# Kernel tuning notes

Measured on AMD Instinct MI355X. Metric: run time of the kernel, lower is better.

## Reference

```python
import jax, jax.numpy as jnp
import numpy as np

NUM_QUBITS = 12
NUM_LAYERS = 2
STATE_DIM = 2 ** NUM_QUBITS
BATCH = 4096
TWO_PI = 2 * 3.1416  # matches the original initializer constant


def _u3(theta, phi, lam):
    """Single-qubit U3 gate, 2x2 complex64 (matches TF layer exactly)."""
    c = jnp.cos(theta / 2)
    s = jnp.sin(theta / 2)
    z = jnp.zeros_like(phi)
    e_phi = jnp.exp(jax.lax.complex(z, phi))
    e_lam = jnp.exp(jax.lax.complex(z, lam))
    e_pl = jnp.exp(jax.lax.complex(z, phi + lam))
    cc = jax.lax.complex(c, jnp.zeros_like(c))
    sc = jax.lax.complex(s, jnp.zeros_like(s))
    row1 = jnp.stack([cc, -e_lam * sc])
    row2 = jnp.stack([e_phi * sc, e_pl * cc])
    return jnp.stack([row1, row2])  # [2, 2] complex64


def _full_gate(theta_vec, phi_vec, lam_vec):
    """Kronecker product of per-qubit gates -> [2^n, 2^n] complex64."""
    full = _u3(theta_vec[0], phi_vec[0], lam_vec[0])
    for q in range(1, theta_vec.shape[0]):
        full = jnp.kron(full, _u3(theta_vec[q], phi_vec[q], lam_vec[q]))
    return full


def setup_inputs() -> dict:
    key = jax.random.key(0)
    k1, k2, k3, k4 = jax.random.split(key, 4)
    inputs = jax.random.normal(k1, (BATCH, STATE_DIM), dtype=jnp.float32)
    thetas = jax.random.uniform(k2, (NUM_LAYERS, NUM_QUBITS), minval=0.0, maxval=TWO_PI, dtype=jnp.float32)
    phis = jax.random.uniform(k3, (NUM_LAYERS, NUM_QUBITS), minval=0.0, maxval=TWO_PI, dtype=jnp.float32)
    lams = jax.random.uniform(k4, (NUM_LAYERS, NUM_QUBITS), minval=0.0, maxval=TWO_PI, dtype=jnp.float32)
    return {"inputs": inputs, "thetas": thetas, "phis": phis, "lams": lams}


def reference(inputs, thetas, phis, lams):
    # normalize real inputs as complex state, per-sample L2 norm
    state = jax.lax.complex(inputs, jnp.zeros_like(inputs))  # [B, D] complex64
    norm = jnp.linalg.norm(state, axis=1, keepdims=True)      # real, [B, 1]
    state = state / norm
    for l in range(thetas.shape[0]):
        U = _full_gate(thetas[l], phis[l], lams[l])  # [D, D]
        # matvec(U, x) per sample == state @ U^T, batched GEMM replaces tf.map_fn
        state = state @ U.T
    return jnp.real(state * jnp.conj(state))  # probabilities, [B, D] float32
```

## Files before the change

kernel.cpp:

```cpp
#include <hip/hip_runtime.h>
#include <hip/hip_fp16.h>

#define NQ   12
#define DIM  4096
#define NL   2
#define BATCH 4096

typedef _Float16 half8  __attribute__((ext_vector_type(8)));
typedef float    f32x16 __attribute__((ext_vector_type(16)));
typedef __fp16   hv2    __attribute__((ext_vector_type(2)));


union U4H8 { uint4 u; half8 h; };

__device__ __forceinline__ unsigned pkrtz(float a, float b) {
    union { hv2 h; unsigned u; } c;
    c.h = __builtin_amdgcn_cvt_pkrtz(a, b);
    return c.u;
}

__global__ void build_gates(const float* __restrict__ th,
                            const float* __restrict__ ph,
                            const float* __restrict__ lm,
                            unsigned short* __restrict__ ws) {
    __shared__ float g[12][8];
    int t = threadIdx.x;
    if (t < NQ) {
        int q = t;
        float g00r = 1.f, g00i = 0.f, g01r = 0.f, g01i = 0.f;
        float g10r = 0.f, g10i = 0.f, g11r = 1.f, g11i = 0.f;
        #pragma unroll
        for (int l = 0; l < NL; ++l) {
            float th2 = 0.5f * th[l * NQ + q];
            float p   = ph[l * NQ + q];
            float la  = lm[l * NQ + q];
            float s, c, sl, cl, sp, cp, spl, cpl;
            sincosf(th2, &s, &c);
            sincosf(la, &sl, &cl);
            sincosf(p, &sp, &cp);
            sincosf(p + la, &spl, &cpl);
            float u00r = c,        u00i = 0.f;
            float u01r = -cl * s,  u01i = -sl * s;
            float u10r = cp * s,   u10i = sp * s;
            float u11r = cpl * c,  u11i = spl * c;
            float n00r = u00r*g00r - u00i*g00i + u01r*g10r - u01i*g10i;
            float n00i = u00r*g00i + u00i*g00r + u01r*g10i + u01i*g10r;
            float n01r = u00r*g01r - u00i*g01i + u01r*g11r - u01i*g11i;
            float n01i = u00r*g01i + u00i*g01r + u01r*g11i + u01i*g11r;
            float n10r = u10r*g00r - u10i*g00i + u11r*g10r - u11i*g10i;
            float n10i = u10r*g00i + u10i*g00r + u11r*g10i + u11i*g10r;
            float n11r = u10r*g01r - u10i*g01i + u11r*g11r - u11i*g11i;
            float n11i = u10r*g01i + u10i*g01r + u11r*g11i + u11i*g11r;
            g00r = n00r; g00i = n00i; g01r = n01r; g01i = n01i;
            g10r = n10r; g10i = n10i; g11r = n11r; g11i = n11i;
        }
        g[q][0] = g00r; g[q][1] = g00i; g[q][2] = g01r; g[q][3] = g01i;
        g[q][4] = g10r; g[q][5] = g10i; g[q][6] = g11r; g[q][7] = g11i;
    }
    __syncthreads();

    for (int idx = t; idx < 24576; idx += 256) {
        int arr  = idx >> 13;
        int rem  = idx & 8191;
        int frag = rem >> 9;
        int lane = (rem >> 3) & 63;
        int j    = rem & 7;
        int row, col, base, k, nn = 0;
        if (arr == 0) {
            int n4 = frag >> 2, ks = frag & 3;
            nn  = n4 * 32 + (lane & 31);
            k   = ks * 16 + ((lane >> 5) << 3) + j;
            row = nn & 63; col = k; base = 6;
        } else {
            int m = frag >> 3, ks = frag & 7;
            row = m * 32 + (lane & 31);
            k   = ks * 16 + ((lane >> 5) << 3) + j;
            col = k & 63; base = 0;
        }
        float re = 1.f, im = 0.f;
        #pragma unroll
        for (int qq = 0; qq < 6; ++qq) {
            const float* G = g[base + qq];
            int rb = (row >> (5 - qq)) & 1;
            int cb = (col >> (5 - qq)) & 1;
            float fr = G[rb * 4 + cb * 2], fi = G[rb * 4 + cb * 2 + 1];
            float nre = re * fr - im * fi;
            float nim = re * fi + im * fr;
            re = nre; im = nim;
        }
        float val;
        if (arr == 0)      val = (nn < 64) ? re : im;
        else if (arr == 1) val = (k < 64) ? re : -im;
        else               val = (k < 64) ? im :  re;
        union { __fp16 h; unsigned short s; } cv;
        cv.h = (__fp16)val;
        ws[idx] = cv.s;
    }
}

__global__ __launch_bounds__(256, 2)
void qc_sim(const float* __restrict__ in,
            const unsigned short* __restrict__ gw,
            float* __restrict__ out) {
    __shared__ unsigned Xh32[2048];
    __shared__ unsigned Tc32[4096];
    __shared__ float red[4];

    const int t = threadIdx.x, lane = t & 63, w = t >> 6, b = blockIdx.x;
    const int m1 = w & 1, ng = (w >> 1) * 2;
    const int m2 = w & 1, n2 = w >> 1;

    const uint4* __restrict__ wsv = reinterpret_cast<const uint4*>(gw);
    uint4 g1b[2][4], m1f[8], m2f[8];
    #pragma unroll
    for (int n = 0; n < 2; ++n)
        #pragma unroll
        for (int ks = 0; ks < 4; ++ks)
            g1b[n][ks] = wsv[((ng + n) * 4 + ks) * 64 + lane];
    #pragma unroll
    for (int ks = 0; ks < 8; ++ks) m1f[ks] = wsv[1024 + (m2 * 8 + ks) * 64 + lane];
    #pragma unroll
    for (int ks = 0; ks < 8; ++ks) m2f[ks] = wsv[2048 + (m2 * 8 + ks) * 64 + lane];

    const float4* __restrict__ x4 =
        reinterpret_cast<const float4*>(in + (size_t)b * DIM);
    float4 lX[4];
    #pragma unroll
    for (int j = 0; j < 4; ++j) lX[j] = x4[j * 256 + t];

    float ss = 0.f;
    #pragma unroll
    for (int j = 0; j < 4; ++j)
        ss += lX[j].x*lX[j].x + lX[j].y*lX[j].y + lX[j].z*lX[j].z + lX[j].w*lX[j].w;
    #pragma unroll
    for (int off = 32; off > 0; off >>= 1) ss += __shfl_down(ss, off, 64);
    if (lane == 0) red[w] = ss;

    #pragma unroll
    for (int j = 0; j < 4; ++j) {
        int fi = (j * 256 + t) * 4, r = fi >> 6, c = fi & 63;
        int a32 = r * 32 + ((((c >> 3) ^ (r & 7)) << 2)) + ((c & 7) >> 1);
        Xh32[a32]     = pkrtz(lX[j].x, lX[j].y);
        Xh32[a32 + 1] = pkrtz(lX[j].z, lX[j].w);
    }
    __syncthreads();
    const float inv = 1.0f / (red[0] + red[1] + red[2] + red[3]);

    f32x16 acc0 = {0,0,0,0,0,0,0,0,0,0,0,0,0,0,0,0};
    f32x16 acc1 = {0,0,0,0,0,0,0,0,0,0,0,0,0,0,0,0};
    const int rowX = m1 * 32 + (lane & 31);
    #pragma unroll
    for (int ks = 0; ks < 4; ++ks) {
        int kb  = ks * 16 + ((lane >> 5) << 3);
        int a32 = rowX * 32 + ((((kb >> 3) ^ (rowX & 7)) << 2));
        U4H8 xf; xf.u = *reinterpret_cast<const uint4*>(&Xh32[a32]);
        U4H8 b0; b0.u = g1b[0][ks];
        U4H8 b1; b1.u = g1b[1][ks];
        acc0 = __builtin_amdgcn_mfma_f32_32x32x16_f16(xf.h, b0.h, acc0, 0, 0, 0);
        acc1 = __builtin_amdgcn_mfma_f32_32x32x16_f16(xf.h, b1.h, acc1, 0, 0, 0);
    }

    #pragma unroll
    for (int tile = 0; tile < 2; ++tile) {
        int nt = ng + tile;
        const f32x16& acc = tile ? acc1 : acc0;
        int kofs = m1 * 32 + 64 * (nt >> 1) + ((lane >> 5) << 2);
        int cc   = (nt & 1) * 32 + (lane & 31);
        #pragma unroll
        for (int p = 0; p < 4; ++p) {
            int k0  = kofs + p * 8;
            int a32 = cc * 64 + (((k0 >> 3) ^ (cc & 15)) << 2) + ((k0 & 7) >> 1);
            Tc32[a32]     = pkrtz(acc[4 * p],     acc[4 * p + 1]);
            Tc32[a32 + 1] = pkrtz(acc[4 * p + 2], acc[4 * p + 3]);
        }
    }
    __syncthreads();

    f32x16 accR = {0,0,0,0,0,0,0,0,0,0,0,0,0,0,0,0};
    f32x16 accI = {0,0,0,0,0,0,0,0,0,0,0,0,0,0,0,0};
    const int cT = n2 * 32 + (lane & 31);
    #pragma unroll
    for (int ks = 0; ks < 8; ++ks) {
        int kb  = ks * 16 + ((lane >> 5) << 3);
        int a32 = cT * 64 + (((kb >> 3) ^ (cT & 15)) << 2);
        U4H8 tf; tf.u = *reinterpret_cast<const uint4*>(&Tc32[a32]);
        U4H8 a1; a1.u = m1f[ks];
        U4H8 a2; a2.u = m2f[ks];
        accR = __builtin_amdgcn_mfma_f32_32x32x16_f16(a1.h, tf.h, accR, 0, 0, 0);
        accI = __builtin_amdgcn_mfma_f32_32x32x16_f16(a2.h, tf.h, accI, 0, 0, 0);
    }

    float* __restrict__ o = out + (size_t)b * DIM
        + (size_t)((m2 * 32 + ((lane >> 5) << 2)) * 64 + n2 * 32 + (lane & 31));
    #pragma unroll
    for (int r = 0; r < 16; ++r) {
        int off = ((r & 3) + 8 * (r >> 2)) * 64;
        o[off] = (accR[r] * accR[r] + accI[r] * accI[r]) * inv;
    }
}

extern "C" void kernel_launch(void* const* d_in, const int* in_sizes, int n_in,
                              void* d_out, int out_size, void* d_ws, size_t ws_size,
                              hipStream_t stream) {
    (void)in_sizes; (void)n_in; (void)out_size; (void)ws_size;
    const float* inputs = (const float*)d_in[0];
    const float* thetas = (const float*)d_in[1];
    const float* phis   = (const float*)d_in[2];
    const float* lams   = (const float*)d_in[3];
    unsigned short* gates = (unsigned short*)d_ws;
    float* out = (float*)d_out;

    hipLaunchKernelGGL(build_gates, dim3(1), dim3(256), 0, stream,
                       thetas, phis, lams, gates);
    hipLaunchKernelGGL(qc_sim, dim3(BATCH), dim3(256), 0, stream,
                       inputs, gates, out);
}
```

Measured before the change: 137.8 us.

## Process eight samples per block with input prefetch; parallelize gate-fragment construction

Each qc_sim block now loops over eight batch samples. The gate MFMA fragments are loaded into registers once per block instead of once per sample, and the next sample's input is prefetched while the current one is computed. build_gates now runs 96 blocks, each writing one fragment element per thread instead of one block looping serially. In exchange, the grid drops to 512 blocks, which leaves fewer resident waves per CU for latency hiding. Every gate block also recomputes the small per-qubit gate table redundantly.

Result: faster. 123.5 us (-10.4%).

```diff
diff --git a/kernel.cpp b/kernel.cpp
--- a/kernel.cpp
+++ b/kernel.cpp
@@ -5,6 +5,7 @@
 #define DIM  4096
 #define NL   2
 #define BATCH 4096
+#define SPB  8
 
 typedef _Float16 half8  __attribute__((ext_vector_type(8)));
 typedef float    f32x16 __attribute__((ext_vector_type(16)));
@@ -59,7 +60,8 @@
     }
     __syncthreads();
 
-    for (int idx = t; idx < 24576; idx += 256) {
+    {
+        int idx  = blockIdx.x * 256 + t;
         int arr  = idx >> 13;
         int rem  = idx & 8191;
         int frag = rem >> 9;
@@ -122,80 +124,98 @@
     #pragma unroll
     for (int ks = 0; ks < 8; ++ks) m2f[ks] = wsv[2048 + (m2 * 8 + ks) * 64 + lane];
 
-    const float4* __restrict__ x4 =
-        reinterpret_cast<const float4*>(in + (size_t)b * DIM);
-    float4 lX[4];
-    #pragma unroll
-    for (int j = 0; j < 4; ++j) lX[j] = x4[j * 256 + t];
-
-    float ss = 0.f;
-    #pragma unroll
-    for (int j = 0; j < 4; ++j)
-        ss += lX[j].x*lX[j].x + lX[j].y*lX[j].y + lX[j].z*lX[j].z + lX[j].w*lX[j].w;
-    #pragma unroll
-    for (int off = 32; off > 0; off >>= 1) ss += __shfl_down(ss, off, 64);
-    if (lane == 0) red[w] = ss;
-
-    #pragma unroll
-    for (int j = 0; j < 4; ++j) {
-        int fi = (j * 256 + t) * 4, r = fi >> 6, c = fi & 63;
-        int a32 = r * 32 + ((((c >> 3) ^ (r & 7)) << 2)) + ((c & 7) >> 1);
-        Xh32[a32]     = pkrtz(lX[j].x, lX[j].y);
-        Xh32[a32 + 1] = pkrtz(lX[j].z, lX[j].w);
-    }
-    __syncthreads();
-    const float inv = 1.0f / (red[0] + red[1] + red[2] + red[3]);
-
-    f32x16 acc0 = {0,0,0,0,0,0,0,0,0,0,0,0,0,0,0,0};
-    f32x16 acc1 = {0,0,0,0,0,0,0,0,0,0,0,0,0,0,0,0};
-    const int rowX = m1 * 32 + (lane & 31);
-    #pragma unroll
-    for (int ks = 0; ks < 4; ++ks) {
-        int kb  = ks * 16 + ((lane >> 5) << 3);
-        int a32 = rowX * 32 + ((((kb >> 3) ^ (rowX & 7)) << 2));
-        U4H8 xf; xf.u = *reinterpret_cast<const uint4*>(&Xh32[a32]);
-        U4H8 b0; b0.u = g1b[0][ks];
-        U4H8 b1; b1.u = g1b[1][ks];
-        acc0 = __builtin_amdgcn_mfma_f32_32x32x16_f16(xf.h, b0.h, acc0, 0, 0, 0);
-        acc1 = __builtin_amdgcn_mfma_f32_32x32x16_f16(xf.h, b1.h, acc1, 0, 0, 0);
-    }
-
-    #pragma unroll
-    for (int tile = 0; tile < 2; ++tile) {
-        int nt = ng + tile;
-        const f32x16& acc = tile ? acc1 : acc0;
-        int kofs = m1 * 32 + 64 * (nt >> 1) + ((lane >> 5) << 2);
-        int cc   = (nt & 1) * 32 + (lane & 31);
-        #pragma unroll
-        for (int p = 0; p < 4; ++p) {
-            int k0  = kofs + p * 8;
-            int a32 = cc * 64 + (((k0 >> 3) ^ (cc & 15)) << 2) + ((k0 & 7) >> 1);
-            Tc32[a32]     = pkrtz(acc[4 * p],     acc[4 * p + 1]);
-            Tc32[a32 + 1] = pkrtz(acc[4 * p + 2], acc[4 * p + 3]);
-        }
-    }
-    __syncthreads();
-
-    f32x16 accR = {0,0,0,0,0,0,0,0,0,0,0,0,0,0,0,0};
-    f32x16 accI = {0,0,0,0,0,0,0,0,0,0,0,0,0,0,0,0};
-    const int cT = n2 * 32 + (lane & 31);
-    #pragma unroll
-    for (int ks = 0; ks < 8; ++ks) {
-        int kb  = ks * 16 + ((lane >> 5) << 3);
-        int a32 = cT * 64 + (((kb >> 3) ^ (cT & 15)) << 2);
-        U4H8 tf; tf.u = *reinterpret_cast<const uint4*>(&Tc32[a32]);
-        U4H8 a1; a1.u = m1f[ks];
-        U4H8 a2; a2.u = m2f[ks];
-        accR = __builtin_amdgcn_mfma_f32_32x32x16_f16(a1.h, tf.h, accR, 0, 0, 0);
-        accI = __builtin_amdgcn_mfma_f32_32x32x16_f16(a2.h, tf.h, accI, 0, 0, 0);
-    }
-
-    float* __restrict__ o = out + (size_t)b * DIM
-        + (size_t)((m2 * 32 + ((lane >> 5) << 2)) * 64 + n2 * 32 + (lane & 31));
-    #pragma unroll
-    for (int r = 0; r < 16; ++r) {
-        int off = ((r & 3) + 8 * (r >> 2)) * 64;
-        o[off] = (accR[r] * accR[r] + accI[r] * accI[r]) * inv;
+    const float* __restrict__ base_in  = in  + (size_t)b * SPB * DIM;
+    float*       __restrict__ base_out = out + (size_t)b * SPB * DIM;
+
+    float4 cur[4], nxt[4];
+    {
+        const float4* __restrict__ x4 = reinterpret_cast<const float4*>(base_in);
+        #pragma unroll
+        for (int j = 0; j < 4; ++j) cur[j] = x4[j * 256 + t];
+    }
+
+    for (int s = 0; s < SPB; ++s) {
+        float ss = 0.f;
+        #pragma unroll
+        for (int j = 0; j < 4; ++j)
+            ss += cur[j].x*cur[j].x + cur[j].y*cur[j].y
+                + cur[j].z*cur[j].z + cur[j].w*cur[j].w;
+        #pragma unroll
+        for (int off = 32; off > 0; off >>= 1) ss += __shfl_down(ss, off, 64);
+        if (lane == 0) red[w] = ss;
+
+        #pragma unroll
+        for (int j = 0; j < 4; ++j) {
+            int fi = (j * 256 + t) * 4, r = fi >> 6, c = fi & 63;
+            int a32 = r * 32 + ((((c >> 3) ^ (r & 7)) << 2)) + ((c & 7) >> 1);
+            Xh32[a32]     = pkrtz(cur[j].x, cur[j].y);
+            Xh32[a32 + 1] = pkrtz(cur[j].z, cur[j].w);
+        }
+        if (s + 1 < SPB) {
+            const float4* __restrict__ xn =
+                reinterpret_cast<const float4*>(base_in + (size_t)(s + 1) * DIM);
+            #pragma unroll
+            for (int j = 0; j < 4; ++j) nxt[j] = xn[j * 256 + t];
+        }
+        __syncthreads();
+        const float inv = 1.0f / (red[0] + red[1] + red[2] + red[3]);
+
+        f32x16 acc0 = {0,0,0,0,0,0,0,0,0,0,0,0,0,0,0,0};
+        f32x16 acc1 = {0,0,0,0,0,0,0,0,0,0,0,0,0,0,0,0};
+        const int rowX = m1 * 32 + (lane & 31);
+        #pragma unroll
+        for (int ks = 0; ks < 4; ++ks) {
+            int kb  = ks * 16 + ((lane >> 5) << 3);
+            int a32 = rowX * 32 + ((((kb >> 3) ^ (rowX & 7)) << 2));
+            U4H8 xf; xf.u = *reinterpret_cast<const uint4*>(&Xh32[a32]);
+            U4H8 b0; b0.u = g1b[0][ks];
+            U4H8 b1; b1.u = g1b[1][ks];
+            acc0 = __builtin_amdgcn_mfma_f32_32x32x16_f16(xf.h, b0.h, acc0, 0, 0, 0);
+            acc1 = __builtin_amdgcn_mfma_f32_32x32x16_f16(xf.h, b1.h, acc1, 0, 0, 0);
+        }
+
+        #pragma unroll
+        for (int tile = 0; tile < 2; ++tile) {
+            int nt = ng + tile;
+            const f32x16& acc = tile ? acc1 : acc0;
+            int kofs = m1 * 32 + 64 * (nt >> 1) + ((lane >> 5) << 2);
+            int cc   = (nt & 1) * 32 + (lane & 31);
+            #pragma unroll
+            for (int p = 0; p < 4; ++p) {
+                int k0  = kofs + p * 8;
+                int a32 = cc * 64 + (((k0 >> 3) ^ (cc & 15)) << 2) + ((k0 & 7) >> 1);
+                Tc32[a32]     = pkrtz(acc[4 * p],     acc[4 * p + 1]);
+                Tc32[a32 + 1] = pkrtz(acc[4 * p + 2], acc[4 * p + 3]);
+            }
+        }
+        __syncthreads();
+
+        f32x16 accR = {0,0,0,0,0,0,0,0,0,0,0,0,0,0,0,0};
+        f32x16 accI = {0,0,0,0,0,0,0,0,0,0,0,0,0,0,0,0};
+        const int cT = n2 * 32 + (lane & 31);
+        #pragma unroll
+        for (int ks = 0; ks < 8; ++ks) {
+            int kb  = ks * 16 + ((lane >> 5) << 3);
+            int a32 = cT * 64 + (((kb >> 3) ^ (cT & 15)) << 2);
+            U4H8 tf; tf.u = *reinterpret_cast<const uint4*>(&Tc32[a32]);
+            U4H8 a1; a1.u = m1f[ks];
+            U4H8 a2; a2.u = m2f[ks];
+            accR = __builtin_amdgcn_mfma_f32_32x32x16_f16(a1.h, tf.h, accR, 0, 0, 0);
+            accI = __builtin_amdgcn_mfma_f32_32x32x16_f16(a2.h, tf.h, accI, 0, 0, 0);
+        }
+
+        float* __restrict__ o = base_out + (size_t)s * DIM
+            + (size_t)((m2 * 32 + ((lane >> 5) << 2)) * 64 + n2 * 32 + (lane & 31));
+        #pragma unroll
+        for (int r = 0; r < 16; ++r) {
+            int off = ((r & 3) + 8 * (r >> 2)) * 64;
+            o[off] = (accR[r] * accR[r] + accI[r] * accI[r]) * inv;
+        }
+
+        if (s + 1 < SPB) {
+            #pragma unroll
+            for (int j = 0; j < 4; ++j) cur[j] = nxt[j];
+        }
     }
 }
 
@@ -210,8 +230,8 @@
     unsigned short* gates = (unsigned short*)d_ws;
     float* out = (float*)d_out;
 
-    hipLaunchKernelGGL(build_gates, dim3(1), dim3(256), 0, stream,
+    hipLaunchKernelGGL(build_gates, dim3(96), dim3(256), 0, stream,
                        thetas, phis, lams, gates);
-    hipLaunchKernelGGL(qc_sim, dim3(BATCH), dim3(256), 0, stream,
+    hipLaunchKernelGGL(qc_sim, dim3(BATCH / SPB), dim3(256), 0, stream,
                        inputs, gates, out);
 }
```
